# Kernel optimization log

Measured on AMD Instinct MI355X. Metric: run time of the kernel, lower is better.

The kernel has to match this reference:

```python
import jax, jax.numpy as jnp
import numpy as np

ALPHA = 0.2  # LeakyReLU negative slope


def setup_inputs() -> dict:
    key = jax.random.key(0)
    k1, k2, k3, k4 = jax.random.split(key, 4)
    N, Fin, Fout = 8192, 256, 64
    inputs = {
        "input": jax.random.normal(k1, (N, Fin), dtype=jnp.float32),
        "adj": jax.random.randint(k2, (N, N), 0, 2, dtype=jnp.int32),
        "W": jax.random.normal(k3, (Fin, Fout), dtype=jnp.float32) * (1.414 * np.sqrt(2.0 / (Fin + Fout))),
        "a": jax.random.normal(k4, (2 * Fout, 1), dtype=jnp.float32) * (1.414 * np.sqrt(2.0 / (2 * Fout + 1))),
    }
    return inputs


def reference(input, adj, W, a):
    # h: [N, Fout]
    h = input @ W
    Fout = h.shape[1]
    # Decompose pairwise score: e[i,j] = leakyrelu(h[i]@a1 + h[j]@a2)
    # (mathematically identical to the original concat+matmul construction,
    #  but avoids the O(N^2 * 2F) intermediate)
    a1, a2 = a[:Fout, 0], a[Fout:, 0]
    s1 = h @ a1  # [N]
    s2 = h @ a2  # [N]
    e = jax.nn.leaky_relu(s1[:, None] + s2[None, :], negative_slope=ALPHA)  # [N, N]
    # Mask non-edges with -10 (as in the original), row softmax
    masked = jnp.where(adj > 0, e, jnp.float32(-10.0))
    attention = jax.nn.softmax(masked, axis=1)
    # dropout p=0.0 (eval/reference mode): identity
    h_prime = attention @ h  # [N, Fout]
    return jax.nn.elu(h_prime)  # concat=True path
```

## Files before the change

kernel.cpp:

```cpp
#include <hip/hip_runtime.h>
#include <hip/hip_bf16.h>
#include <cstdint>
#include <cstddef>

#define NN 8192
#define FIN 256
#define FOUT 64
#define ALPHA_SLOPE 0.2f
#define EXP_M10 4.5399929762484854e-05f

#define JSPLIT 16
#define KITER 16
#define CP 68

typedef short s16x8 __attribute__((ext_vector_type(8)));
typedef float f32x4 __attribute__((ext_vector_type(4)));
typedef int   i32x4 __attribute__((ext_vector_type(4)));
typedef float f32x4v __attribute__((ext_vector_type(4)));

__device__ __forceinline__ unsigned short f2bf(float x) {
    union { float f; uint32_t u; } v; v.f = x;
    uint32_t u = v.u;
    return (unsigned short)((u + 0x7FFFu + ((u >> 16) & 1u)) >> 16);
}

__global__ __launch_bounds__(256) void k_h(
    const float* __restrict__ input, const float* __restrict__ W,
    const float* __restrict__ a,
    unsigned short* __restrict__ htg, float* __restrict__ s1, float* __restrict__ s2)
{
    __shared__ __align__(16) unsigned short tile[64][28];
    const int wid  = threadIdx.x >> 6;
    const int lane = threadIdx.x & 63;
    const int i0   = blockIdx.x * 16;
    const int r0   = wid * 4;
    const float* inb = input + (size_t)(i0 + r0) * FIN;

    float acc0 = 0.f, acc1 = 0.f, acc2 = 0.f, acc3 = 0.f;
    #pragma unroll 4
    for (int c = 0; c < FIN; c += 4) {
        float w0 = W[(c + 0) * FOUT + lane];
        float w1 = W[(c + 1) * FOUT + lane];
        float w2 = W[(c + 2) * FOUT + lane];
        float w3 = W[(c + 3) * FOUT + lane];
        float4 x0 = *(const float4*)(inb + 0 * FIN + c);
        float4 x1 = *(const float4*)(inb + 1 * FIN + c);
        float4 x2 = *(const float4*)(inb + 2 * FIN + c);
        float4 x3 = *(const float4*)(inb + 3 * FIN + c);
        acc0 = fmaf(x0.x, w0, fmaf(x0.y, w1, fmaf(x0.z, w2, fmaf(x0.w, w3, acc0))));
        acc1 = fmaf(x1.x, w0, fmaf(x1.y, w1, fmaf(x1.z, w2, fmaf(x1.w, w3, acc1))));
        acc2 = fmaf(x2.x, w0, fmaf(x2.y, w1, fmaf(x2.z, w2, fmaf(x2.w, w3, acc2))));
        acc3 = fmaf(x3.x, w0, fmaf(x3.y, w1, fmaf(x3.z, w2, fmaf(x3.w, w3, acc3))));
    }

    const float a1v = a[lane], a2v = a[FOUT + lane];
    float accs[4] = {acc0, acc1, acc2, acc3};
    #pragma unroll
    for (int r = 0; r < 4; ++r) {
        float v1 = accs[r] * a1v;
        float v2 = accs[r] * a2v;
        #pragma unroll
        for (int off = 32; off; off >>= 1) {
            v1 += __shfl_xor(v1, off);
            v2 += __shfl_xor(v2, off);
        }
        if (lane == 0) { s1[i0 + r0 + r] = v1; s2[i0 + r0 + r] = v2; }
        tile[lane][r0 + r] = f2bf(accs[r]);
    }
    __syncthreads();

    const int feat = threadIdx.x >> 2;
    const int cg   = (threadIdx.x & 3) * 4;
    uint2 q = *(const uint2*)&tile[feat][cg];
    *(uint2*)(htg + (size_t)feat * NN + i0 + cg) = q;
}

__global__ __launch_bounds__(256, 4) void k_attn(
    const int* __restrict__ adj,
    const unsigned short* __restrict__ htg,
    const float* __restrict__ s1g, const float* __restrict__ s2g,
    float* __restrict__ slabs)
{
    const int t    = threadIdx.x;
    const int wid  = t >> 6;
    const int lane = t & 63;
    const int gw   = blockIdx.x * 4 + wid;
    const int mi   = gw >> 4;
    const int js   = gw & 15;
    const int m    = lane & 15;
    const int quad = lane >> 4;
    const int irow = mi * 16 + m;
    const int jb   = js * (NN / JSPLIT) + quad * 8;

    const float s1v = s1g[irow];

    const short bd = (m == 0) ? (short)0x3F80 : (short)0;
    const s16x8 bden = {bd, bd, bd, bd, bd, bd, bd, bd};

    f32x4 acc0 = {0,0,0,0}, acc1 = {0,0,0,0}, acc2 = {0,0,0,0},
          acc3 = {0,0,0,0}, acc4 = {0,0,0,0};

    const int*   aptr = adj + (size_t)irow * NN + jb;
    const float* s2p  = s2g + jb;
    const unsigned short* h0 = htg + (size_t)(m +  0) * NN + jb;
    const unsigned short* h1 = htg + (size_t)(m + 16) * NN + jb;
    const unsigned short* h2 = htg + (size_t)(m + 32) * NN + jb;
    const unsigned short* h3 = htg + (size_t)(m + 48) * NN + jb;

    #pragma unroll
    for (int ko = 0; ko < KITER; ++ko) {
        const int o = ko * 32;
        i32x4  av0 = __builtin_nontemporal_load((const i32x4*)(aptr + o));
        i32x4  av1 = __builtin_nontemporal_load((const i32x4*)(aptr + o + 4));
        float4 sa  = *(const float4*)(s2p + o);
        float4 sb  = *(const float4*)(s2p + o + 4);
        s16x8  b0  = *(const s16x8*)(h0 + o);
        s16x8  b1  = *(const s16x8*)(h1 + o);
        s16x8  b2  = *(const s16x8*)(h2 + o);
        s16x8  b3  = *(const s16x8*)(h3 + o);

        float x0 = s1v + sa.x, x1 = s1v + sa.y, x2 = s1v + sa.z, x3 = s1v + sa.w;
        float x4 = s1v + sb.x, x5 = s1v + sb.y, x6 = s1v + sb.z, x7 = s1v + sb.w;
        float w0 = (av0.x > 0) ? __expf(fmaxf(x0, ALPHA_SLOPE * x0)) : EXP_M10;
        float w1 = (av0.y > 0) ? __expf(fmaxf(x1, ALPHA_SLOPE * x1)) : EXP_M10;
        float w2 = (av0.z > 0) ? __expf(fmaxf(x2, ALPHA_SLOPE * x2)) : EXP_M10;
        float w3 = (av0.w > 0) ? __expf(fmaxf(x3, ALPHA_SLOPE * x3)) : EXP_M10;
        float w4 = (av1.x > 0) ? __expf(fmaxf(x4, ALPHA_SLOPE * x4)) : EXP_M10;
        float w5 = (av1.y > 0) ? __expf(fmaxf(x5, ALPHA_SLOPE * x5)) : EXP_M10;
        float w6 = (av1.z > 0) ? __expf(fmaxf(x6, ALPHA_SLOPE * x6)) : EXP_M10;
        float w7 = (av1.w > 0) ? __expf(fmaxf(x7, ALPHA_SLOPE * x7)) : EXP_M10;

        s16x8 af;
        af[0] = (short)f2bf(w0); af[1] = (short)f2bf(w1);
        af[2] = (short)f2bf(w2); af[3] = (short)f2bf(w3);
        af[4] = (short)f2bf(w4); af[5] = (short)f2bf(w5);
        af[6] = (short)f2bf(w6); af[7] = (short)f2bf(w7);

        acc0 = __builtin_amdgcn_mfma_f32_16x16x32_bf16(af, b0,   acc0, 0, 0, 0);
        acc1 = __builtin_amdgcn_mfma_f32_16x16x32_bf16(af, b1,   acc1, 0, 0, 0);
        acc2 = __builtin_amdgcn_mfma_f32_16x16x32_bf16(af, b2,   acc2, 0, 0, 0);
        acc3 = __builtin_amdgcn_mfma_f32_16x16x32_bf16(af, b3,   acc3, 0, 0, 0);
        acc4 = __builtin_amdgcn_mfma_f32_16x16x32_bf16(af, bden, acc4, 0, 0, 0);
    }

    float* slab = slabs + (size_t)js * ((size_t)NN * CP);
    const int r0 = mi * 16 + quad * 4;
    #pragma unroll
    for (int reg = 0; reg < 4; ++reg) {
        size_t ro = (size_t)(r0 + reg) * CP;
        slab[ro +  0 + m] = acc0[reg];
        slab[ro + 16 + m] = acc1[reg];
        slab[ro + 32 + m] = acc2[reg];
        slab[ro + 48 + m] = acc3[reg];
        if (m == 0) slab[ro + 64] = acc4[reg];
    }
}

__global__ __launch_bounds__(256) void k_norm(
    const float* __restrict__ slabs, float* __restrict__ out)
{
    int gid = blockIdx.x * 256 + threadIdx.x;
    int i = gid >> 6, k = gid & 63;
    float num = 0.f, den = 0.f;
    #pragma unroll
    for (int js = 0; js < JSPLIT; ++js) {
        const float* row = slabs + (size_t)js * ((size_t)NN * CP) + (size_t)i * CP;
        num += row[k];
        den += row[64];
    }
    float v = num / den;
    out[gid] = (v > 0.f) ? v : (__expf(v) - 1.f);
}

extern "C" void kernel_launch(void* const* d_in, const int* in_sizes, int n_in,
                              void* d_out, int out_size, void* d_ws, size_t ws_size,
                              hipStream_t stream) {
    const float* input = (const float*)d_in[0];
    const int*   adj   = (const int*)d_in[1];
    const float* W     = (const float*)d_in[2];
    const float* a     = (const float*)d_in[3];
    float* out = (float*)d_out;

    char* ws = (char*)d_ws;
    float* slabs = (float*)ws;
    size_t off = (size_t)JSPLIT * NN * CP * sizeof(float);
    unsigned short* htg = (unsigned short*)(ws + off);
    off += (size_t)FOUT * NN * sizeof(unsigned short);
    float* s1 = (float*)(ws + off); off += NN * sizeof(float);
    float* s2 = (float*)(ws + off);

    k_h   <<<NN / 16, 256, 0, stream>>>(input, W, a, htg, s1, s2);
    k_attn<<<(NN / 16) * JSPLIT / 4, 256, 0, stream>>>(adj, htg, s1, s2, slabs);
    k_norm<<<NN * FOUT / 256, 256, 0, stream>>>(slabs, out);
}
```

Before: 459.7 us.

## Stage attention weights through LDS with coalesced adjacency loads and fewer J-splits

Restructures the attention kernel so each block's four waves cooperatively load 16 adjacency rows with coalesced vector loads, compute bf16 softmax weights into a swizzled shared-memory tile, then split the K range across waves for MFMA accumulation. Partial results are reduced in shared memory before writing. JSPLIT is reduced from 16 to 2, shrinking slab writes and the final normalization reads. It adds block-wide barriers per tile and drops non-temporal hints, and the smaller grid may reduce parallelism.

Measured after the change: 443.6 us. -3.5%, faster.

```diff
diff --git a/kernel.cpp b/kernel.cpp
--- a/kernel.cpp
+++ b/kernel.cpp
@@ -9,19 +9,23 @@
 #define ALPHA_SLOPE 0.2f
 #define EXP_M10 4.5399929762484854e-05f
 
-#define JSPLIT 16
-#define KITER 16
+#define JSPLIT 2
+#define JT 1024
+#define NTILE ((NN / JSPLIT) / JT)
 #define CP 68
 
 typedef short s16x8 __attribute__((ext_vector_type(8)));
 typedef float f32x4 __attribute__((ext_vector_type(4)));
 typedef int   i32x4 __attribute__((ext_vector_type(4)));
-typedef float f32x4v __attribute__((ext_vector_type(4)));
 
 __device__ __forceinline__ unsigned short f2bf(float x) {
     union { float f; uint32_t u; } v; v.f = x;
     uint32_t u = v.u;
     return (unsigned short)((u + 0x7FFFu + ((u >> 16) & 1u)) >> 16);
+}
+
+__device__ __forceinline__ int wt_off(int row, int chunk) {
+    return row * JT + (((chunk) ^ (row & 7)) << 3);
 }
 
 __global__ __launch_bounds__(256) void k_h(
@@ -81,18 +85,24 @@
     const float* __restrict__ s1g, const float* __restrict__ s2g,
     float* __restrict__ slabs)
 {
+    __shared__ __align__(16) unsigned short Wt[16 * JT];
+
     const int t    = threadIdx.x;
     const int wid  = t >> 6;
     const int lane = t & 63;
-    const int gw   = blockIdx.x * 4 + wid;
-    const int mi   = gw >> 4;
-    const int js   = gw & 15;
+    const int bi   = blockIdx.x >> 1;
+    const int js   = blockIdx.x & 1;
+    const int i0   = bi * 16;
+    const int jbase = js * (NN / JSPLIT);
     const int m    = lane & 15;
     const int quad = lane >> 4;
-    const int irow = mi * 16 + m;
-    const int jb   = js * (NN / JSPLIT) + quad * 8;
-
-    const float s1v = s1g[irow];
+
+    const int srow = wid * 4;
+    float s1r[4];
+    #pragma unroll
+    for (int r = 0; r < 4; ++r) s1r[r] = s1g[i0 + srow + r];
+
+    const int kq = wid * (JT / 4);
 
     const short bd = (m == 0) ? (short)0x3F80 : (short)0;
     const s16x8 bden = {bd, bd, bd, bd, bd, bd, bd, bd};
@@ -100,59 +110,72 @@
     f32x4 acc0 = {0,0,0,0}, acc1 = {0,0,0,0}, acc2 = {0,0,0,0},
           acc3 = {0,0,0,0}, acc4 = {0,0,0,0};
 
-    const int*   aptr = adj + (size_t)irow * NN + jb;
-    const float* s2p  = s2g + jb;
-    const unsigned short* h0 = htg + (size_t)(m +  0) * NN + jb;
-    const unsigned short* h1 = htg + (size_t)(m + 16) * NN + jb;
-    const unsigned short* h2 = htg + (size_t)(m + 32) * NN + jb;
-    const unsigned short* h3 = htg + (size_t)(m + 48) * NN + jb;
-
-    #pragma unroll
-    for (int ko = 0; ko < KITER; ++ko) {
-        const int o = ko * 32;
-        i32x4  av0 = __builtin_nontemporal_load((const i32x4*)(aptr + o));
-        i32x4  av1 = __builtin_nontemporal_load((const i32x4*)(aptr + o + 4));
-        float4 sa  = *(const float4*)(s2p + o);
-        float4 sb  = *(const float4*)(s2p + o + 4);
-        s16x8  b0  = *(const s16x8*)(h0 + o);
-        s16x8  b1  = *(const s16x8*)(h1 + o);
-        s16x8  b2  = *(const s16x8*)(h2 + o);
-        s16x8  b3  = *(const s16x8*)(h3 + o);
-
-        float x0 = s1v + sa.x, x1 = s1v + sa.y, x2 = s1v + sa.z, x3 = s1v + sa.w;
-        float x4 = s1v + sb.x, x5 = s1v + sb.y, x6 = s1v + sb.z, x7 = s1v + sb.w;
-        float w0 = (av0.x > 0) ? __expf(fmaxf(x0, ALPHA_SLOPE * x0)) : EXP_M10;
-        float w1 = (av0.y > 0) ? __expf(fmaxf(x1, ALPHA_SLOPE * x1)) : EXP_M10;
-        float w2 = (av0.z > 0) ? __expf(fmaxf(x2, ALPHA_SLOPE * x2)) : EXP_M10;
-        float w3 = (av0.w > 0) ? __expf(fmaxf(x3, ALPHA_SLOPE * x3)) : EXP_M10;
-        float w4 = (av1.x > 0) ? __expf(fmaxf(x4, ALPHA_SLOPE * x4)) : EXP_M10;
-        float w5 = (av1.y > 0) ? __expf(fmaxf(x5, ALPHA_SLOPE * x5)) : EXP_M10;
-        float w6 = (av1.z > 0) ? __expf(fmaxf(x6, ALPHA_SLOPE * x6)) : EXP_M10;
-        float w7 = (av1.w > 0) ? __expf(fmaxf(x7, ALPHA_SLOPE * x7)) : EXP_M10;
-
-        s16x8 af;
-        af[0] = (short)f2bf(w0); af[1] = (short)f2bf(w1);
-        af[2] = (short)f2bf(w2); af[3] = (short)f2bf(w3);
-        af[4] = (short)f2bf(w4); af[5] = (short)f2bf(w5);
-        af[6] = (short)f2bf(w6); af[7] = (short)f2bf(w7);
-
-        acc0 = __builtin_amdgcn_mfma_f32_16x16x32_bf16(af, b0,   acc0, 0, 0, 0);
-        acc1 = __builtin_amdgcn_mfma_f32_16x16x32_bf16(af, b1,   acc1, 0, 0, 0);
-        acc2 = __builtin_amdgcn_mfma_f32_16x16x32_bf16(af, b2,   acc2, 0, 0, 0);
-        acc3 = __builtin_amdgcn_mfma_f32_16x16x32_bf16(af, b3,   acc3, 0, 0, 0);
-        acc4 = __builtin_amdgcn_mfma_f32_16x16x32_bf16(af, bden, acc4, 0, 0, 0);
-    }
+    for (int tile = 0; tile < NTILE; ++tile) {
+        const int j0 = jbase + tile * JT;
+        __syncthreads();
+
+        #pragma unroll
+        for (int rr = 0; rr < 4; ++rr) {
+            const int row = srow + rr;
+            const int* ap = adj + (size_t)(i0 + row) * NN + j0;
+            const float s1v = s1r[rr];
+            #pragma unroll
+            for (int c = 0; c < 4; ++c) {
+                const int cc = c * 256 + lane * 4;
+                i32x4  av = *(const i32x4*)(ap + cc);
+                float4 sv = *(const float4*)(s2g + j0 + cc);
+                float x0 = s1v + sv.x, x1 = s1v + sv.y;
+                float x2 = s1v + sv.z, x3 = s1v + sv.w;
+                float w0 = (av.x > 0) ? __expf(fmaxf(x0, ALPHA_SLOPE * x0)) : EXP_M10;
+                float w1 = (av.y > 0) ? __expf(fmaxf(x1, ALPHA_SLOPE * x1)) : EXP_M10;
+                float w2 = (av.z > 0) ? __expf(fmaxf(x2, ALPHA_SLOPE * x2)) : EXP_M10;
+                float w3 = (av.w > 0) ? __expf(fmaxf(x3, ALPHA_SLOPE * x3)) : EXP_M10;
+                uint2 pk;
+                pk.x = (unsigned int)f2bf(w0) | ((unsigned int)f2bf(w1) << 16);
+                pk.y = (unsigned int)f2bf(w2) | ((unsigned int)f2bf(w3) << 16);
+                const int chunk = c * 32 + (lane >> 1);
+                *(uint2*)&Wt[wt_off(row, chunk) + (lane & 1) * 4] = pk;
+            }
+        }
+        __syncthreads();
+
+        #pragma unroll
+        for (int ks = 0; ks < 8; ++ks) {
+            const int kc = kq + ks * 32;
+            s16x8 af = *(const s16x8*)&Wt[wt_off(m, (kc >> 3) + quad)];
+            const unsigned short* hp = htg + (size_t)m * NN + j0 + kc + quad * 8;
+            s16x8 b0 = *(const s16x8*)(hp);
+            s16x8 b1 = *(const s16x8*)(hp + (size_t)16 * NN);
+            s16x8 b2 = *(const s16x8*)(hp + (size_t)32 * NN);
+            s16x8 b3 = *(const s16x8*)(hp + (size_t)48 * NN);
+            acc0 = __builtin_amdgcn_mfma_f32_16x16x32_bf16(af, b0,   acc0, 0, 0, 0);
+            acc1 = __builtin_amdgcn_mfma_f32_16x16x32_bf16(af, b1,   acc1, 0, 0, 0);
+            acc2 = __builtin_amdgcn_mfma_f32_16x16x32_bf16(af, b2,   acc2, 0, 0, 0);
+            acc3 = __builtin_amdgcn_mfma_f32_16x16x32_bf16(af, b3,   acc3, 0, 0, 0);
+            acc4 = __builtin_amdgcn_mfma_f32_16x16x32_bf16(af, bden, acc4, 0, 0, 0);
+        }
+    }
+
+    __syncthreads();
+    float* red = (float*)Wt;
+    float* myred = red + wid * 16 * CP;
+    #pragma unroll
+    for (int reg = 0; reg < 4; ++reg) {
+        const int r = quad * 4 + reg;
+        myred[r * CP +  0 + m] = acc0[reg];
+        myred[r * CP + 16 + m] = acc1[reg];
+        myred[r * CP + 32 + m] = acc2[reg];
+        myred[r * CP + 48 + m] = acc3[reg];
+        if (m == 0) myred[r * CP + 64] = acc4[reg];
+    }
+    __syncthreads();
 
     float* slab = slabs + (size_t)js * ((size_t)NN * CP);
-    const int r0 = mi * 16 + quad * 4;
-    #pragma unroll
-    for (int reg = 0; reg < 4; ++reg) {
-        size_t ro = (size_t)(r0 + reg) * CP;
-        slab[ro +  0 + m] = acc0[reg];
-        slab[ro + 16 + m] = acc1[reg];
-        slab[ro + 32 + m] = acc2[reg];
-        slab[ro + 48 + m] = acc3[reg];
-        if (m == 0) slab[ro + 64] = acc4[reg];
+    for (int idx = t; idx < 16 * 65; idx += 256) {
+        const int r = idx / 65, c = idx % 65;
+        float s = red[0 * 16 * CP + r * CP + c] + red[1 * 16 * CP + r * CP + c]
+                + red[2 * 16 * CP + r * CP + c] + red[3 * 16 * CP + r * CP + c];
+        slab[(size_t)(i0 + r) * CP + c] = s;
     }
 }
 
@@ -190,6 +213,6 @@
     float* s2 = (float*)(ws + off);
 
     k_h   <<<NN / 16, 256, 0, stream>>>(input, W, a, htg, s1, s2);
-    k_attn<<<(NN / 16) * JSPLIT / 4, 256, 0, stream>>>(adj, htg, s1, s2, slabs);
+    k_attn<<<(NN / 16) * JSPLIT, 256, 0, stream>>>(adj, htg, s1, s2, slabs);
     k_norm<<<NN * FOUT / 256, 256, 0, stream>>>(slabs, out);
 }
```
